# Optimization experiments

Measured on AMD Instinct MI355X. Metric: run time of the kernel, lower is better.

## Reference

```python
import jax, jax.numpy as jnp
import numpy as np

B, N, C = 8, 1024, 768
H = 12
D = C // H  # head_dim = 64
SCALE = D ** -0.5
EPS = 1e-5


def _layer_norm(x):
    # per-head LayerNorm over last dim, gamma=1, beta=0, biased variance
    mean = x.mean(-1, keepdims=True)
    var = ((x - mean) ** 2).mean(-1, keepdims=True)
    return (x - mean) / jnp.sqrt(var + EPS)


def setup_inputs() -> dict:
    key = jax.random.key(0)
    k1, k2, k3 = jax.random.split(key, 3)
    x = jax.random.normal(k1, (B, N, C), dtype=jnp.float32)
    qkv_weight = jax.random.normal(k2, (3 * C, C), dtype=jnp.float32) * (C ** -0.5)
    proj_weight = jax.random.normal(k3, (C, C), dtype=jnp.float32) * (C ** -0.5)
    return {"x": x, "qkv_weight": qkv_weight, "proj_weight": proj_weight}


def reference(x, qkv_weight, proj_weight):
    Bx, Nx, Cx = x.shape
    qkv = x @ qkv_weight.T                          # [B,N,3C]
    qkv = qkv.reshape(Bx, Nx, 3, H, D).transpose(2, 0, 3, 1, 4)  # [3,B,H,N,D]
    q, k, v = qkv[0], qkv[1], qkv[2]
    q = _layer_norm(q) * SCALE
    k = _layer_norm(k)
    attn = jnp.einsum('bhnd,bhmd->bhnm', q, k)      # [B,H,N,N]
    attn = jax.nn.softmax(attn, axis=-1)
    out = jnp.einsum('bhnm,bhmd->bhnd', attn, v)    # [B,H,N,D]
    out = out.transpose(0, 2, 1, 3).reshape(Bx, Nx, Cx)
    return out @ proj_weight.T
```

## Files before the change

### kernel.cpp

```cpp
#include <hip/hip_runtime.h>
#include <stdint.h>
#include <stddef.h>

#define HB 8
#define HN 1024
#define HC 768
#define HH 12
#define HD 64
#define ROWS (HB*HN)
#define BH (HB*HH)

using s16x4  = __attribute__((ext_vector_type(4))) short;
using bf16x8 = __attribute__((ext_vector_type(8))) short;
using f32x4  = __attribute__((ext_vector_type(4))) float;

__device__ __forceinline__ short f2bf(float f) {
  union { float f; uint32_t u; } c; c.f = f;
  uint32_t u = c.u;
  uint32_t r = (u + 0x7fffu + ((u >> 16) & 1u)) >> 16;
  return (short)r;
}
__device__ __forceinline__ float bf2f(short s) {
  union { uint32_t u; float f; } c; c.u = ((uint32_t)(uint16_t)s) << 16;
  return c.f;
}
__device__ __forceinline__ uint32_t pack_bf16_rne(float a, float b) {
  union { float f; uint32_t u; } ca, cb; ca.f = a; cb.f = b;
  uint32_t ra = ca.u + 0x7fffu + ((ca.u >> 16) & 1u);
  uint32_t rb = cb.u + 0x7fffu + ((cb.u >> 16) & 1u);
  return __builtin_amdgcn_perm(rb, ra, 0x07060302);
}
__device__ __forceinline__ float fast_exp2(float x) {
#if __has_builtin(__builtin_amdgcn_exp2f)
  return __builtin_amdgcn_exp2f(x);
#else
  return exp2f(x);
#endif
}
__device__ __forceinline__ f32x4 mfma16(bf16x8 a, bf16x8 b, f32x4 c) {
  return __builtin_amdgcn_mfma_f32_16x16x32_bf16(a, b, c, 0, 0, 0);
}
__device__ __forceinline__ void gll16(const void* g, void* l) {
  __builtin_amdgcn_global_load_lds((const __attribute__((address_space(1))) void*)g,
                                   (__attribute__((address_space(3))) void*)l,
                                   16, 0, 0);
}

__global__ void cvt3_kernel(const float* __restrict__ x,  short* __restrict__ xb,  int n0,
                            const float* __restrict__ wq, short* __restrict__ wqb, int n1,
                            const float* __restrict__ wp, short* __restrict__ wpb, int n2) {
  int i = blockIdx.x * 256 + threadIdx.x;
  const float* in; short* out;
  if (i < n0)            { in = x;  out = xb;  }
  else if (i < n0 + n1)  { i -= n0; in = wq; out = wqb; }
  else if (i < n0 + n1 + n2) { i -= n0 + n1; in = wp; out = wpb; }
  else return;
  float4 v = ((const float4*)in)[i];
  s16x4 o;
  o.x = f2bf(v.x); o.y = f2bf(v.y); o.z = f2bf(v.z); o.w = f2bf(v.w);
  ((s16x4*)out)[i] = o;
}

__device__ __forceinline__ void store_c(float* p, float v) { *p = v; }
__device__ __forceinline__ void store_c(short* p, float v) { *p = f2bf(v); }

template<int VM, bool STG, int SLOT>
__device__ __forceinline__ void qkv_ktile(
    int kt, short* sA, short* sB,
    const short* Ag, const short* Bg,
    int wr, int wc, int quad, int lc,
    int aoff0, int aoff1, int boff0,
    int cA0, int cA1, int cB0,
    f32x4 (&acc)[4][4])
{
  if constexpr (VM == 3) asm volatile("s_waitcnt vmcnt(3)" ::: "memory");
  else                   asm volatile("s_waitcnt vmcnt(0)" ::: "memory");
  __builtin_amdgcn_s_barrier();
  if constexpr (STG) {
    constexpr int DST = (SLOT + 2) % 3;
    const int kcol = (kt + 2) * 32;
    short* dA = sA + DST*8192;
    short* dB = sB + DST*4096;
    gll16(Ag + (size_t)(aoff0 + kcol), (void*)(dA + cA0*8));
    gll16(Ag + (size_t)(aoff1 + kcol), (void*)(dA + cA1*8));
    gll16(Bg + (size_t)(boff0 + kcol), (void*)(dB + cB0*8));
  }
  const short* sa = sA + SLOT*8192;
  const short* sb = sB + SLOT*4096;
  bf16x8 af[4], bfr[4];
#pragma unroll
  for (int mt = 0; mt < 4; ++mt) {
    const int rA = wr*64 + mt*16 + lc;
    af[mt] = *(const bf16x8*)(sa + rA*32 + (quad ^ ((rA >> 1) & 3))*8);
  }
#pragma unroll
  for (int nt = 0; nt < 4; ++nt) {
    const int rB = wc*64 + nt*16 + lc;
    bfr[nt] = *(const bf16x8*)(sb + rB*32 + (quad ^ ((rB >> 1) & 3))*8);
  }
  __builtin_amdgcn_s_setprio(1);
#pragma unroll
  for (int mt = 0; mt < 4; ++mt)
#pragma unroll
    for (int nt = 0; nt < 4; ++nt)
      acc[mt][nt] = mfma16(af[mt], bfr[nt], acc[mt][nt]);
  __builtin_amdgcn_s_setprio(0);
}

__global__ __launch_bounds__(512, 4) void gemm_qkv(const short* __restrict__ A,
                                                   const short* __restrict__ Bw,
                                                   short* __restrict__ Qb,
                                                   short* __restrict__ Kb,
                                                   short* __restrict__ Vtb) {
  __shared__ short SMEM[3*256*32 + 3*128*32];
  short* As = SMEM;
  short* Bs = SMEM + 3*256*32;
  const int wg = blockIdx.x;
  const int swz = (wg & 7)*72 + (wg >> 3);
  const int by = swz / 18, bx = swz % 18;
  const int m0 = by*256, n0 = bx*128;
  const int tid = threadIdx.x;
  const int lane = tid & 63, w = tid >> 6, quad = lane >> 4, lc = lane & 15;
  const int wr = w >> 1, wc = w & 1;
  const int cA0 = tid,        rA0 = cA0 >> 2, sbA0 = ((cA0 & 3) ^ ((rA0 >> 1) & 3))*8;
  const int cA1 = 512 + tid,  rA1 = cA1 >> 2, sbA1 = ((cA1 & 3) ^ ((rA1 >> 1) & 3))*8;
  const int cB0 = tid,        rB0 = cB0 >> 2, sbB0 = ((cB0 & 3) ^ ((rB0 >> 1) & 3))*8;
  const int aoff0 = rA0*HC + sbA0;
  const int aoff1 = rA1*HC + sbA1;
  const int boff0 = rB0*HC + sbB0;
  const short* Ag = A  + (size_t)m0*HC;
  const short* Bg = Bw + (size_t)n0*HC;
  f32x4 acc[4][4] = {};

#pragma unroll
  for (int pk = 0; pk < 2; ++pk) {
    gll16(Ag + (size_t)(aoff0 + pk*32), (void*)(As + pk*8192 + cA0*8));
    gll16(Ag + (size_t)(aoff1 + pk*32), (void*)(As + pk*8192 + cA1*8));
    gll16(Bg + (size_t)(boff0 + pk*32), (void*)(Bs + pk*4096 + cB0*8));
  }

#pragma unroll 1
  for (int kt = 0; kt < 21; kt += 3) {
    qkv_ktile<3,true,0>(kt,   As, Bs, Ag, Bg, wr, wc, quad, lc,
                        aoff0, aoff1, boff0, cA0, cA1, cB0, acc);
    qkv_ktile<3,true,1>(kt+1, As, Bs, Ag, Bg, wr, wc, quad, lc,
                        aoff0, aoff1, boff0, cA0, cA1, cB0, acc);
    qkv_ktile<3,true,2>(kt+2, As, Bs, Ag, Bg, wr, wc, quad, lc,
                        aoff0, aoff1, boff0, cA0, cA1, cB0, acc);
  }
  qkv_ktile<3,true ,0>(21, As, Bs, Ag, Bg, wr, wc, quad, lc,
                       aoff0, aoff1, boff0, cA0, cA1, cB0, acc);
  qkv_ktile<3,false,1>(22, As, Bs, Ag, Bg, wr, wc, quad, lc,
                       aoff0, aoff1, boff0, cA0, cA1, cB0, acc);
  qkv_ktile<0,false,2>(23, As, Bs, Ag, Bg, wr, wc, quad, lc,
                       aoff0, aoff1, boff0, cA0, cA1, cB0, acc);

  const int cg = n0 + wc*64;
  const int t = cg / HC;
  const int h = (cg % HC) / HD;
  if (t < 2) {
    short* outp = (t == 0) ? Qb : Kb;
    const float sc = (t == 0) ? 0.125f : 1.0f;
#pragma unroll
    for (int i = 0; i < 4; ++i)
#pragma unroll
      for (int r = 0; r < 4; ++r) {
        float s1 = (acc[i][0][r] + acc[i][1][r]) + (acc[i][2][r] + acc[i][3][r]);
        float s2 = acc[i][0][r]*acc[i][0][r];
        s2 = __builtin_fmaf(acc[i][1][r], acc[i][1][r], s2);
        s2 = __builtin_fmaf(acc[i][2][r], acc[i][2][r], s2);
        s2 = __builtin_fmaf(acc[i][3][r], acc[i][3][r], s2);
#pragma unroll
        for (int off = 1; off < 16; off <<= 1) {
          s1 += __shfl_xor(s1, off);
          s2 += __shfl_xor(s2, off);
        }
        const float mean = s1 * (1.0f/64.0f);
        const float var  = s2 * (1.0f/64.0f) - mean*mean;
        const float inv  = rsqrtf(var + 1e-5f) * sc;
        const int row = m0 + wr*64 + i*16 + quad*4 + r;
        const int b = row >> 10, n_in = row & 1023;
        short* rowp = outp + ((size_t)(b*HH + h)*HN + n_in)*HD;
#pragma unroll
        for (int nt = 0; nt < 4; ++nt)
          rowp[nt*16 + lc] = f2bf((acc[i][nt][r] - mean) * inv);
      }
  } else {
    short* vs = SMEM;
    __syncthreads();
    const int hd = wc;
#pragma unroll
    for (int i = 0; i < 4; ++i)
#pragma unroll
      for (int nt = 0; nt < 4; ++nt)
#pragma unroll
        for (int r = 0; r < 4; ++r) {
          const int dd = nt*16 + lc;
          const int k  = i*16 + quad*4 + r;
          const int c  = ((k & 15) << 2) | (k >> 4);
          vs[(hd*64 + dd)*268 + wr*64 + c] = f2bf(acc[i][nt][r]);
        }
    __syncthreads();
    const int b = m0 >> 10, m0g = m0 & 1023;
#pragma unroll
    for (int it = 0; it < 8; ++it) {
      const int idx = it*512 + tid;
      const int h2 = idx >> 11;
      const int rem = idx & 2047;
      const int dd = rem >> 5, c8 = rem & 31;
      const int habs = ((n0 + h2*64) - 1536) >> 6;
      const short* src = vs + (h2*64 + dd)*268 + c8*8;
      s16x4 lo = *(const s16x4*)(src);
      s16x4 hi = *(const s16x4*)(src + 4);
      bf16x8 vvv;
      vvv[0]=lo[0]; vvv[1]=lo[1]; vvv[2]=lo[2]; vvv[3]=lo[3];
      vvv[4]=hi[0]; vvv[5]=hi[1]; vvv[6]=hi[2]; vvv[7]=hi[3];
      *(bf16x8*)(Vtb + ((size_t)((b*HH + habs)*HD + dd))*HN + m0g + c8*8) = vvv;
    }
  }
}

__global__ __launch_bounds__(256) void gemm_bt_f32(const short* __restrict__ A,
                                                   const short* __restrict__ Bw,
                                                   float* __restrict__ C,
                                                   int M, int N, int K) {
  __shared__ short As[128*64];
  __shared__ short Bs[128*64];
  const int m0 = blockIdx.y * 128, n0 = blockIdx.x * 128;
  const int tid = threadIdx.x;
  const int lane = tid & 63, w = tid >> 6, quad = lane >> 4, lc = lane & 15;
  const int wr = w >> 1, wc = w & 1;
  f32x4 acc[4][4] = {};
  for (int kt = 0; kt < K; kt += 64) {
#pragma unroll
    for (int i = 0; i < 4; ++i) {
      const int chunk = i*256 + tid;
      const int r = chunk >> 3, cb = chunk & 7;
      const int cbs = cb ^ (r & 7);
      gll16(A  + (size_t)(m0 + r)*K + kt + cbs*8, (void*)(As + (size_t)chunk*8));
      gll16(Bw + (size_t)(n0 + r)*K + kt + cbs*8, (void*)(Bs + (size_t)chunk*8));
    }
    __syncthreads();
#pragma unroll
    for (int kk = 0; kk < 2; ++kk) {
      bf16x8 af[4], bfr[4];
      const int kb = kk*4 + quad;
#pragma unroll
      for (int mt = 0; mt < 4; ++mt)
        af[mt] = *(const bf16x8*)(As + (wr*64 + mt*16 + lc)*64 + (kb ^ (lc & 7))*8);
#pragma unroll
      for (int nt = 0; nt < 4; ++nt)
        bfr[nt] = *(const bf16x8*)(Bs + (wc*64 + nt*16 + lc)*64 + (kb ^ (lc & 7))*8);
#pragma unroll
      for (int mt = 0; mt < 4; ++mt)
#pragma unroll
        for (int nt = 0; nt < 4; ++nt)
          acc[mt][nt] = mfma16(af[mt], bfr[nt], acc[mt][nt]);
    }
    __syncthreads();
  }
#pragma unroll
  for (int mt = 0; mt < 4; ++mt)
#pragma unroll
    for (int nt = 0; nt < 4; ++nt)
#pragma unroll
      for (int r = 0; r < 4; ++r) {
        const int row = m0 + wr*64 + mt*16 + quad*4 + r;
        const int col = n0 + wc*64 + nt*16 + lc;
        store_c(C + (size_t)row*N + col, acc[mt][nt][r]);
      }
}

__global__ __launch_bounds__(256, 3) void attn_kernel(const short* __restrict__ Qb,
                                                      const short* __restrict__ Kb,
                                                      const short* __restrict__ Vtb,
                                                      short* __restrict__ AOb) {
  const int raw = blockIdx.x;
  const int blk = (raw & 7)*96 + (raw >> 3);
  const int qt = blk & 7, bh = blk >> 3;
  const int b = bh / HH, h = bh % HH;
  const int tid = threadIdx.x, w = tid >> 6, lane = tid & 63;
  const int quad = lane >> 4, lc = lane & 15;

  __shared__ short Ks [64][72];
  __shared__ short Vts[64][72];
  __shared__ short Ps [4][32][72];

  bf16x8 aq[2][2];
#pragma unroll
  for (int mt = 0; mt < 2; ++mt) {
    const int mrow = qt*128 + w*32 + mt*16 + lc;
    aq[mt][0] = *(const bf16x8*)(Qb + ((size_t)bh*HN + mrow)*HD + quad*8);
    aq[mt][1] = *(const bf16x8*)(Qb + ((size_t)bh*HN + mrow)*HD + 32 + quad*8);
  }

  const short* kbh = Kb  + (size_t)bh*HN*HD;
  const short* vbh = Vtb + (size_t)bh*HD*HN;

  f32x4 oacc[2][4] = {};
  float l_i[2][4] = {};

  bf16x8 gk[2], gv[2];
#pragma unroll
  for (int i = 0; i < 2; ++i) {
    const int c = i*256 + tid;
    gk[i] = *(const bf16x8*)(kbh + (size_t)(c >> 3)*HD + (c & 7)*8);
    gv[i] = *(const bf16x8*)(vbh + (size_t)(c >> 3)*HN + (c & 7)*8);
  }
#pragma unroll
  for (int i = 0; i < 2; ++i) {
    const int c = i*256 + tid;
    *(bf16x8*)(&Ks [c >> 3][(c & 7)*8]) = gk[i];
    *(bf16x8*)(&Vts[c >> 3][(c & 7)*8]) = gv[i];
  }
  __syncthreads();

  const float LOG2E = 1.44269504f;
  const float MB2   = 8.0f * 1.44269504f;

  for (int ck = 0; ck < 16; ++ck) {
    if (ck < 15) {
      const int nn0 = (ck + 1)*64;
#pragma unroll
      for (int i = 0; i < 2; ++i) {
        const int c = i*256 + tid;
        gk[i] = *(const bf16x8*)(kbh + (size_t)(nn0 + (c >> 3))*HD + (c & 7)*8);
        gv[i] = *(const bf16x8*)(vbh + (size_t)(c >> 3)*HN + nn0 + (c & 7)*8);
      }
    }

    f32x4 sacc[2][4] = {};
#pragma unroll
    for (int kk = 0; kk < 2; ++kk)
#pragma unroll
      for (int nt = 0; nt < 4; ++nt) {
        bf16x8 bk = *(const bf16x8*)(&Ks[nt*16 + lc][kk*32 + quad*8]);
#pragma unroll
        for (int mt = 0; mt < 2; ++mt)
          sacc[mt][nt] = mfma16(aq[mt][kk], bk, sacc[mt][nt]);
      }

#pragma unroll
    for (int mt = 0; mt < 2; ++mt)
#pragma unroll
      for (int r = 0; r < 4; ++r) {
        float ps[4];
#pragma unroll
        for (int nt = 0; nt < 4; ++nt) {
          ps[nt] = fast_exp2(__builtin_fmaf(sacc[mt][nt][r], LOG2E, -MB2));
          sacc[mt][nt][r] = ps[nt];
        }
        l_i[mt][r] += (ps[0] + ps[1]) + (ps[2] + ps[3]);
        uint2 pk;
        pk.x = pack_bf16_rne(ps[0], ps[1]);
        pk.y = pack_bf16_rne(ps[2], ps[3]);
        *(uint2*)(&Ps[w][mt*16 + quad*4 + r][lc*4]) = pk;
      }

#pragma unroll
    for (int kk = 0; kk < 2; ++kk) {
      bf16x8 ap[2];
#pragma unroll
      for (int mt = 0; mt < 2; ++mt)
        ap[mt] = *(const bf16x8*)(&Ps[w][mt*16 + lc][kk*32 + quad*8]);
#pragma unroll
      for (int nt2 = 0; nt2 < 4; ++nt2) {
        bf16x8 bv = *(const bf16x8*)(&Vts[nt2*16 + lc][kk*32 + quad*8]);
#pragma unroll
        for (int mt = 0; mt < 2; ++mt)
          oacc[mt][nt2] = mfma16(ap[mt], bv, oacc[mt][nt2]);
      }
    }

    if (ck < 15) {
      __syncthreads();
#pragma unroll
      for (int i = 0; i < 2; ++i) {
        const int c = i*256 + tid;
        *(bf16x8*)(&Ks [c >> 3][(c & 7)*8]) = gk[i];
        *(bf16x8*)(&Vts[c >> 3][(c & 7)*8]) = gv[i];
      }
      __syncthreads();
    }
  }

#pragma unroll
  for (int mt = 0; mt < 2; ++mt)
#pragma unroll
    for (int r = 0; r < 4; ++r) {
      float l = l_i[mt][r];
#pragma unroll
      for (int off = 1; off < 16; off <<= 1) l += __shfl_xor(l, off);
      const float rl = 1.0f / l;
      const int row = qt*128 + w*32 + mt*16 + quad*4 + r;
#pragma unroll
      for (int nt2 = 0; nt2 < 4; ++nt2) {
        const int d = nt2*16 + lc;
        AOb[((size_t)(b*HN + row))*HC + h*HD + d] = f2bf(oacc[mt][nt2][r] * rl);
      }
    }
}

extern "C" void kernel_launch(void* const* d_in, const int* in_sizes, int n_in,
                              void* d_out, int out_size, void* d_ws, size_t ws_size,
                              hipStream_t stream) {
  const float* x     = (const float*)d_in[0];
  const float* wqkv  = (const float*)d_in[1];
  const float* wproj = (const float*)d_in[2];
  float* out = (float*)d_out;

  char* ws = (char*)d_ws;
  size_t off = 0;
  auto alloc = [&](size_t bytes) -> void* {
    void* p = ws + off; off += (bytes + 255) & ~(size_t)255; return p;
  };
  short* xb     = (short*)alloc((size_t)ROWS*HC*2);
  short* wqkvb  = (short*)alloc((size_t)3*HC*HC*2);
  short* wprojb = (short*)alloc((size_t)HC*HC*2);
  short* Qb     = (short*)alloc((size_t)BH*HN*HD*2);
  short* Kb     = (short*)alloc((size_t)BH*HN*HD*2);
  short* Vtb    = (short*)alloc((size_t)BH*HD*HN*2);
  short* AOb    = (short*)alloc((size_t)ROWS*HC*2);

  { const int n0 = ROWS*HC/4, n1 = 3*HC*HC/4, n2 = HC*HC/4;
    const int tot = n0 + n1 + n2;
    cvt3_kernel<<<(tot + 255)/256, 256, 0, stream>>>(x, xb, n0, wqkv, wqkvb, n1,
                                                     wproj, wprojb, n2); }

  gemm_qkv<<<dim3(576), 512, 0, stream>>>(xb, wqkvb, Qb, Kb, Vtb);
  attn_kernel<<<BH*8, 256, 0, stream>>>(Qb, Kb, Vtb, AOb);
  gemm_bt_f32<<<dim3(HC/128, ROWS/128), 256, 0, stream>>>(AOb, wprojb, out,
                                                          ROWS, HC, HC);
}
```

Baseline: 182.6 us.

## Pipeline projection GEMM with triple-buffered async LDS loads and block swizzle

Rewrites the output projection GEMM so it uses a 3-stage ring of LDS buffers with K-tiles of 32. Loads are issued two tiles ahead and gated with vmcnt waits, replacing the load-then-two-syncthreads loop. It also adds an XCD-aware block-index swizzle, s_setprio around the MFMA bursts, and launch bounds for 3 blocks per CU, with the shapes hardcoded. The aim is to hide global load latency behind MFMA work, at the cost of more LDS per block and code that only handles fixed shapes.

```diff
diff --git a/kernel.cpp b/kernel.cpp
--- a/kernel.cpp
+++ b/kernel.cpp
@@ -60,9 +60,6 @@
   o.x = f2bf(v.x); o.y = f2bf(v.y); o.z = f2bf(v.z); o.w = f2bf(v.w);
   ((s16x4*)out)[i] = o;
 }
-
-__device__ __forceinline__ void store_c(float* p, float v) { *p = v; }
-__device__ __forceinline__ void store_c(short* p, float v) { *p = f2bf(v); }
 
 template<int VM, bool STG, int SLOT>
 __device__ __forceinline__ void qkv_ktile(
@@ -220,45 +217,96 @@
   }
 }
 
-__global__ __launch_bounds__(256) void gemm_bt_f32(const short* __restrict__ A,
-                                                   const short* __restrict__ Bw,
-                                                   float* __restrict__ C,
-                                                   int M, int N, int K) {
-  __shared__ short As[128*64];
-  __shared__ short Bs[128*64];
-  const int m0 = blockIdx.y * 128, n0 = blockIdx.x * 128;
+template<int VM, bool STG, int SLOT>
+__device__ __forceinline__ void bt_ktile(
+    int kt, short* sA, short* sB,
+    const short* Ag, const short* Bg,
+    int wr, int wc, int quad, int lc,
+    int aoff0, int aoff1, int boff0, int boff1,
+    int cA0, int cA1, int cB0, int cB1,
+    f32x4 (&acc)[4][4])
+{
+  if constexpr (VM == 4) asm volatile("s_waitcnt vmcnt(4)" ::: "memory");
+  else                   asm volatile("s_waitcnt vmcnt(0)" ::: "memory");
+  __builtin_amdgcn_s_barrier();
+  if constexpr (STG) {
+    constexpr int DST = (SLOT + 2) % 3;
+    const int kcol = (kt + 2) * 32;
+    short* dA = sA + DST*4096;
+    short* dB = sB + DST*4096;
+    gll16(Ag + (size_t)(aoff0 + kcol), (void*)(dA + cA0*8));
+    gll16(Ag + (size_t)(aoff1 + kcol), (void*)(dA + cA1*8));
+    gll16(Bg + (size_t)(boff0 + kcol), (void*)(dB + cB0*8));
+    gll16(Bg + (size_t)(boff1 + kcol), (void*)(dB + cB1*8));
+  }
+  const short* sa = sA + SLOT*4096;
+  const short* sb = sB + SLOT*4096;
+  bf16x8 af[4], bfr[4];
+#pragma unroll
+  for (int mt = 0; mt < 4; ++mt) {
+    const int rA = wr*64 + mt*16 + lc;
+    af[mt] = *(const bf16x8*)(sa + rA*32 + (quad ^ ((rA >> 1) & 3))*8);
+  }
+#pragma unroll
+  for (int nt = 0; nt < 4; ++nt) {
+    const int rB = wc*64 + nt*16 + lc;
+    bfr[nt] = *(const bf16x8*)(sb + rB*32 + (quad ^ ((rB >> 1) & 3))*8);
+  }
+  __builtin_amdgcn_s_setprio(1);
+#pragma unroll
+  for (int mt = 0; mt < 4; ++mt)
+#pragma unroll
+    for (int nt = 0; nt < 4; ++nt)
+      acc[mt][nt] = mfma16(af[mt], bfr[nt], acc[mt][nt]);
+  __builtin_amdgcn_s_setprio(0);
+}
+
+__global__ __launch_bounds__(256, 3) void gemm_bt_f32(const short* __restrict__ A,
+                                                      const short* __restrict__ Bw,
+                                                      float* __restrict__ C) {
+  __shared__ short As[3*128*32];
+  __shared__ short Bs[3*128*32];
+  const int wg = blockIdx.x;
+  const int swz = (wg & 7)*48 + (wg >> 3);
+  const int by = swz / 6, bx = swz % 6;
+  const int m0 = by*128, n0 = bx*128;
   const int tid = threadIdx.x;
   const int lane = tid & 63, w = tid >> 6, quad = lane >> 4, lc = lane & 15;
   const int wr = w >> 1, wc = w & 1;
+  const int cA0 = tid,        rA0 = cA0 >> 2, sbA0 = ((cA0 & 3) ^ ((rA0 >> 1) & 3))*8;
+  const int cA1 = 256 + tid,  rA1 = cA1 >> 2, sbA1 = ((cA1 & 3) ^ ((rA1 >> 1) & 3))*8;
+  const int aoff0 = rA0*HC + sbA0;
+  const int aoff1 = rA1*HC + sbA1;
+  const int cB0 = cA0, cB1 = cA1;
+  const int boff0 = aoff0, boff1 = aoff1;
+  const short* Ag = A  + (size_t)m0*HC;
+  const short* Bg = Bw + (size_t)n0*HC;
   f32x4 acc[4][4] = {};
-  for (int kt = 0; kt < K; kt += 64) {
-#pragma unroll
-    for (int i = 0; i < 4; ++i) {
-      const int chunk = i*256 + tid;
-      const int r = chunk >> 3, cb = chunk & 7;
-      const int cbs = cb ^ (r & 7);
-      gll16(A  + (size_t)(m0 + r)*K + kt + cbs*8, (void*)(As + (size_t)chunk*8));
-      gll16(Bw + (size_t)(n0 + r)*K + kt + cbs*8, (void*)(Bs + (size_t)chunk*8));
-    }
-    __syncthreads();
-#pragma unroll
-    for (int kk = 0; kk < 2; ++kk) {
-      bf16x8 af[4], bfr[4];
-      const int kb = kk*4 + quad;
-#pragma unroll
-      for (int mt = 0; mt < 4; ++mt)
-        af[mt] = *(const bf16x8*)(As + (wr*64 + mt*16 + lc)*64 + (kb ^ (lc & 7))*8);
-#pragma unroll
-      for (int nt = 0; nt < 4; ++nt)
-        bfr[nt] = *(const bf16x8*)(Bs + (wc*64 + nt*16 + lc)*64 + (kb ^ (lc & 7))*8);
-#pragma unroll
-      for (int mt = 0; mt < 4; ++mt)
-#pragma unroll
-        for (int nt = 0; nt < 4; ++nt)
-          acc[mt][nt] = mfma16(af[mt], bfr[nt], acc[mt][nt]);
-    }
-    __syncthreads();
-  }
+
+#pragma unroll
+  for (int pk = 0; pk < 2; ++pk) {
+    gll16(Ag + (size_t)(aoff0 + pk*32), (void*)(As + pk*4096 + cA0*8));
+    gll16(Ag + (size_t)(aoff1 + pk*32), (void*)(As + pk*4096 + cA1*8));
+    gll16(Bg + (size_t)(boff0 + pk*32), (void*)(Bs + pk*4096 + cB0*8));
+    gll16(Bg + (size_t)(boff1 + pk*32), (void*)(Bs + pk*4096 + cB1*8));
+  }
+
+#pragma unroll 1
+  for (int kt = 0; kt < 21; kt += 3) {
+    bt_ktile<4,true,0>(kt,   As, Bs, Ag, Bg, wr, wc, quad, lc,
+                       aoff0, aoff1, boff0, boff1, cA0, cA1, cB0, cB1, acc);
+    bt_ktile<4,true,1>(kt+1, As, Bs, Ag, Bg, wr, wc, quad, lc,
+                       aoff0, aoff1, boff0, boff1, cA0, cA1, cB0, cB1, acc);
+    bt_ktile<4,true,2>(kt+2, As, Bs, Ag, Bg, wr, wc, quad, lc,
+                       aoff0, aoff1, boff0, boff1, cA0, cA1, cB0, cB1, acc);
+  }
+  bt_ktile<4,true ,0>(21, As, Bs, Ag, Bg, wr, wc, quad, lc,
+                      aoff0, aoff1, boff0, boff1, cA0, cA1, cB0, cB1, acc);
+  bt_ktile<4,false,1>(22, As, Bs, Ag, Bg, wr, wc, quad, lc,
+                      aoff0, aoff1, boff0, boff1, cA0, cA1, cB0, cB1, acc);
+  bt_ktile<0,false,2>(23, As, Bs, Ag, Bg, wr, wc, quad, lc,
+                      aoff0, aoff1, boff0, boff1, cA0, cA1, cB0, cB1, acc);
+
 #pragma unroll
   for (int mt = 0; mt < 4; ++mt)
 #pragma unroll
@@ -267,7 +315,7 @@
       for (int r = 0; r < 4; ++r) {
         const int row = m0 + wr*64 + mt*16 + quad*4 + r;
         const int col = n0 + wc*64 + nt*16 + lc;
-        store_c(C + (size_t)row*N + col, acc[mt][nt][r]);
+        C[(size_t)row*HC + col] = acc[mt][nt][r];
       }
 }
 
@@ -429,6 +477,5 @@
 
   gemm_qkv<<<dim3(576), 512, 0, stream>>>(xb, wqkvb, Qb, Kb, Vtb);
   attn_kernel<<<BH*8, 256, 0, stream>>>(Qb, Kb, Vtb, AOb);
-  gemm_bt_f32<<<dim3(HC/128, ROWS/128), 256, 0, stream>>>(AOb, wprojb, out,
-                                                          ROWS, HC, HC);
-}
+  gemm_bt_f32<<<dim3(384), 256, 0, stream>>>(AOb, wprojb, out);
+}
```

After: 181.0 us, median of 2. No clear change (-0.9%).
